# Optimization experiments

Measured on AMD Instinct MI355X. Metric: run time of the kernel, lower is better.

## Reference

```python
import jax, jax.numpy as jnp
import numpy as np

N_ITERATIONS = 3
N_OUT_CAPS = 10


def squash(t, axis=-2):
    # squash(s) = ||s||^2 * s / ((1 + ||s||^2) * ||s||)
    sqr_norm = jnp.sum(t * t, axis=axis, keepdims=True)
    norm = jnp.sqrt(sqr_norm)
    return sqr_norm * t / ((1.0 + sqr_norm) * norm)


def setup_inputs() -> dict:
    key = jax.random.key(0)
    B, I, O, D = 256, 1152, 10, 16
    u_hat = jax.random.normal(key, (B, I, O, D, 1), dtype=jnp.float32)
    return {"u_hat": u_hat}


def reference(u_hat):
    B = u_hat.shape[0]
    I, O = u_hat.shape[1], u_hat.shape[2]
    # routing logits b: (B, I, O, 1, 1)
    b = jnp.zeros((B, I, O, 1, 1), dtype=u_hat.dtype)
    v = None
    for r in range(N_ITERATIONS):
        c = jax.nn.softmax(b, axis=1)                 # softmax over input capsules
        s = jnp.sum(c * u_hat, axis=1, keepdims=True)  # (B, 1, O, D, 1)
        v = squash(s, axis=-2)
        if r < N_ITERATIONS - 1:
            # u_hat^T @ v: (B,I,O,1,D) @ (B,1,O,D,1) -> (B,I,O,1,1)
            b = b + jnp.matmul(jnp.swapaxes(u_hat, -2, -1), v)
    return v.reshape(B, N_OUT_CAPS, -1)
```

## Files before the change

kernel.cpp:

```cpp
#include <hip/hip_runtime.h>
#include <math.h>

#define N_I 1152
#define N_O 10
#define N_D 16
#define BLK 256
#define KPT 18

__global__ __launch_bounds__(BLK, 4)
void caps_route(const float* __restrict__ u_hat, float* __restrict__ out)
{
    __shared__ float scr_s[4][16];
    __shared__ float scr_e[4];
    __shared__ __align__(16) float vcum[16];

    const int tid  = threadIdx.x;
    const int wave = tid >> 6;
    const int lane = tid & 63;
    const int d4   = tid & 3;
    const int ig   = tid >> 2;

    const int bid = blockIdx.x;
    const int nwg = gridDim.x;
    int wid = bid;
    if ((nwg & 7) == 0) wid = (bid & 7) * (nwg >> 3) + (bid >> 3);
    const int b = wid / N_O;
    const int o = wid - b * N_O;

    const float* gbase = u_hat + (size_t)b * (N_I * N_O * N_D)
                               + (size_t)o * N_D + d4 * 4;

    float4 u[KPT];
    float4 s4 = make_float4(0.f, 0.f, 0.f, 0.f);
    #pragma unroll
    for (int k = 0; k < KPT; ++k) {
        const int i = ig + (k << 6);
        u[k] = *(const float4*)(gbase + (size_t)i * (N_O * N_D));
        s4.x += u[k].x; s4.y += u[k].y;
        s4.z += u[k].z; s4.w += u[k].w;
    }
    if (tid < 16) vcum[tid] = 0.0f;

    float4 vc = make_float4(0.f, 0.f, 0.f, 0.f);

    for (int r = 0; r < 3; ++r) {
        float esum;
        if (r == 0) {
            esum = (float)KPT;
        } else {
            s4 = make_float4(0.f, 0.f, 0.f, 0.f);
            esum = 0.0f;
            #pragma unroll
            for (int k = 0; k < KPT; ++k) {
                float p = u[k].x*vc.x + u[k].y*vc.y + u[k].z*vc.z + u[k].w*vc.w;
                p += __shfl_xor(p, 1);
                p += __shfl_xor(p, 2);
                const float e = __expf(p);
                esum += e;
                s4.x += e*u[k].x; s4.y += e*u[k].y;
                s4.z += e*u[k].z; s4.w += e*u[k].w;
            }
        }
        #pragma unroll
        for (int m = 4; m <= 32; m <<= 1) {
            s4.x += __shfl_xor(s4.x, m);
            s4.y += __shfl_xor(s4.y, m);
            s4.z += __shfl_xor(s4.z, m);
            s4.w += __shfl_xor(s4.w, m);
            esum += __shfl_xor(esum, m);
        }
        if (lane < 4) {
            scr_s[wave][lane*4+0] = s4.x;
            scr_s[wave][lane*4+1] = s4.y;
            scr_s[wave][lane*4+2] = s4.z;
            scr_s[wave][lane*4+3] = s4.w;
            if (lane == 0) scr_e[wave] = esum;
        }
        __syncthreads();
        if (tid < 16) {
            float s = 0.f, et = 0.f;
            #pragma unroll
            for (int w = 0; w < 4; ++w) { s += scr_s[w][tid]; et += scr_e[w]; }
            s /= et;
            float sq = s * s;
            sq += __shfl_xor(sq, 1);
            sq += __shfl_xor(sq, 2);
            sq += __shfl_xor(sq, 4);
            sq += __shfl_xor(sq, 8);
            const float nrm = sqrtf(sq);
            const float v = s * (nrm / (1.0f + sq));
            if (r == 2) out[(size_t)wid * N_D + tid] = v;
            else        vcum[tid] += v;
        }
        __syncthreads();
        if (r < 2) vc = ((const float4*)vcum)[d4];
    }
}

extern "C" void kernel_launch(void* const* d_in, const int* in_sizes, int n_in,
                              void* d_out, int out_size, void* d_ws, size_t ws_size,
                              hipStream_t stream)
{
    const float* u_hat = (const float*)d_in[0];
    float* out = (float*)d_out;
    const int B = in_sizes[0] / (N_I * N_O * N_D);
    hipLaunchKernelGGL(caps_route, dim3(B * N_O), dim3(BLK), 0, stream, u_hat, out);
}
```

Baseline: 35.06 us.

## Compute squash redundantly per thread with double-buffered LDS, dropping second barrier

Every thread now reduces the four wave partials and computes the squash itself, keeping the accumulated v in registers. This removes the serial tid<16 phase, the vcum shared array and the second __syncthreads per iteration, and ping-pong buffers the scratch so the next iteration's writes cannot race with reads. Quad reductions use DPP quad permutes instead of shuffles, and the output is written as a float4. The cost is redundant squash math on all threads and more LDS reads.

```diff
diff --git a/kernel.cpp b/kernel.cpp
--- a/kernel.cpp
+++ b/kernel.cpp
@@ -6,13 +6,22 @@
 #define N_D 16
 #define BLK 256
 #define KPT 18
+#define ROWS (N_O * N_D)
+
+__device__ __forceinline__ float qadd1(float x) {
+    return x + __int_as_float(__builtin_amdgcn_update_dpp(
+        0, __float_as_int(x), 0xB1, 0xF, 0xF, true));
+}
+__device__ __forceinline__ float qadd2(float x) {
+    return x + __int_as_float(__builtin_amdgcn_update_dpp(
+        0, __float_as_int(x), 0x4E, 0xF, 0xF, true));
+}
 
 __global__ __launch_bounds__(BLK, 4)
 void caps_route(const float* __restrict__ u_hat, float* __restrict__ out)
 {
-    __shared__ float scr_s[4][16];
-    __shared__ float scr_e[4];
-    __shared__ __align__(16) float vcum[16];
+    __shared__ float4 scr_s[2][4][4];
+    __shared__ float  scr_e[2][4];
 
     const int tid  = threadIdx.x;
     const int wave = tid >> 6;
@@ -27,34 +36,31 @@
     const int b = wid / N_O;
     const int o = wid - b * N_O;
 
-    const float* gbase = u_hat + (size_t)b * (N_I * N_O * N_D)
-                               + (size_t)o * N_D + d4 * 4;
+    const float* g = u_hat + (size_t)b * (N_I * ROWS) + (size_t)o * N_D
+                   + (size_t)ig * ROWS + (size_t)(d4 << 2);
 
     float4 u[KPT];
     float4 s4 = make_float4(0.f, 0.f, 0.f, 0.f);
     #pragma unroll
     for (int k = 0; k < KPT; ++k) {
-        const int i = ig + (k << 6);
-        u[k] = *(const float4*)(gbase + (size_t)i * (N_O * N_D));
+        u[k] = *(const float4*)(g + (size_t)(k << 6) * ROWS);
         s4.x += u[k].x; s4.y += u[k].y;
         s4.z += u[k].z; s4.w += u[k].w;
     }
-    if (tid < 16) vcum[tid] = 0.0f;
+    float esum = (float)KPT;
+    float4 vc = make_float4(0.f, 0.f, 0.f, 0.f);
+    float4 v4;
 
-    float4 vc = make_float4(0.f, 0.f, 0.f, 0.f);
-
+    #pragma unroll
     for (int r = 0; r < 3; ++r) {
-        float esum;
-        if (r == 0) {
-            esum = (float)KPT;
-        } else {
+        if (r > 0) {
             s4 = make_float4(0.f, 0.f, 0.f, 0.f);
             esum = 0.0f;
             #pragma unroll
             for (int k = 0; k < KPT; ++k) {
                 float p = u[k].x*vc.x + u[k].y*vc.y + u[k].z*vc.z + u[k].w*vc.w;
-                p += __shfl_xor(p, 1);
-                p += __shfl_xor(p, 2);
+                p = qadd1(p);
+                p = qadd2(p);
                 const float e = __expf(p);
                 esum += e;
                 s4.x += e*u[k].x; s4.y += e*u[k].y;
@@ -69,32 +75,34 @@
             s4.w += __shfl_xor(s4.w, m);
             esum += __shfl_xor(esum, m);
         }
+        const int pp = r & 1;
         if (lane < 4) {
-            scr_s[wave][lane*4+0] = s4.x;
-            scr_s[wave][lane*4+1] = s4.y;
-            scr_s[wave][lane*4+2] = s4.z;
-            scr_s[wave][lane*4+3] = s4.w;
-            if (lane == 0) scr_e[wave] = esum;
+            scr_s[pp][wave][lane] = s4;
+            if (lane == 0) scr_e[pp][wave] = esum;
         }
         __syncthreads();
-        if (tid < 16) {
-            float s = 0.f, et = 0.f;
-            #pragma unroll
-            for (int w = 0; w < 4; ++w) { s += scr_s[w][tid]; et += scr_e[w]; }
-            s /= et;
-            float sq = s * s;
-            sq += __shfl_xor(sq, 1);
-            sq += __shfl_xor(sq, 2);
-            sq += __shfl_xor(sq, 4);
-            sq += __shfl_xor(sq, 8);
-            const float nrm = sqrtf(sq);
-            const float v = s * (nrm / (1.0f + sq));
-            if (r == 2) out[(size_t)wid * N_D + tid] = v;
-            else        vcum[tid] += v;
+        float4 st = make_float4(0.f, 0.f, 0.f, 0.f);
+        float et = 0.f;
+        #pragma unroll
+        for (int w = 0; w < 4; ++w) {
+            const float4 t = scr_s[pp][w][d4];
+            st.x += t.x; st.y += t.y; st.z += t.z; st.w += t.w;
+            et += scr_e[pp][w];
         }
-        __syncthreads();
-        if (r < 2) vc = ((const float4*)vcum)[d4];
+        const float inv = 1.0f / et;
+        st.x *= inv; st.y *= inv; st.z *= inv; st.w *= inv;
+        float sq = st.x*st.x + st.y*st.y + st.z*st.z + st.w*st.w;
+        sq = qadd1(sq);
+        sq = qadd2(sq);
+        const float nrm = sqrtf(sq);
+        const float f = nrm / (1.0f + sq);
+        v4.x = st.x*f; v4.y = st.y*f; v4.z = st.z*f; v4.w = st.w*f;
+        if (r < 2) {
+            vc.x += v4.x; vc.y += v4.y; vc.z += v4.z; vc.w += v4.w;
+        }
     }
+    if (tid < 4)
+        *(float4*)(out + (size_t)wid * N_D + (tid << 2)) = v4;
 }
 
 extern "C" void kernel_launch(void* const* d_in, const int* in_sizes, int n_in,
```

Measured after the change: 33.71 us, median of 2. 3.9% less time.
